# Performance work log

Measured on AMD Instinct MI355X. Metric: run time of the kernel, lower is better.

The kernel has to match this reference:

```python
import jax, jax.numpy as jnp
import numpy as np

N = 50000   # nodes
E = 800000  # edges (avg degree 16)
F_IN = 128
D_HID = 128
N_CLASS = 40


def setup_inputs() -> dict:
    key = jax.random.key(0)
    ks = jax.random.split(key, 10)
    s = 0.05
    return {
        "x": jax.random.normal(ks[0], (N, F_IN), jnp.float32),
        "edge_index": jax.random.randint(ks[1], (2, E), 0, N, dtype=jnp.int32),
        "W_in": jax.random.normal(ks[2], (F_IN, D_HID), jnp.float32) * s,
        "b_in": jnp.zeros((D_HID,), jnp.float32),
        "W1": jax.random.normal(ks[3], (D_HID, D_HID), jnp.float32) * s,
        "b1": jnp.zeros((D_HID,), jnp.float32),
        "W2": jax.random.normal(ks[4], (D_HID, D_HID), jnp.float32) * s,
        "b2": jnp.zeros((D_HID,), jnp.float32),
        "W_out": jax.random.normal(ks[5], (D_HID, N_CLASS), jnp.float32) * s,
        "b_out": jnp.zeros((N_CLASS,), jnp.float32),
    }


def _gcn_norm(edge_index, num_nodes):
    # Add self loops, compute symmetric normalization D^-1/2 (A+I) D^-1/2.
    loop = jnp.arange(num_nodes, dtype=edge_index.dtype)
    src = jnp.concatenate([edge_index[0], loop])
    dst = jnp.concatenate([edge_index[1], loop])
    deg = jnp.zeros((num_nodes,), jnp.float32).at[dst].add(1.0)
    dinv = jnp.where(deg > 0, jax.lax.rsqrt(deg), 0.0)
    norm = dinv[src] * dinv[dst]  # [E+N]
    return src, dst, norm


def _gcn_conv(h, W, b, src, dst, norm, num_nodes):
    # transform then sparse aggregate (gather-scale-scatter)
    h = h @ W                                   # [N, d]
    msg = h[src] * norm[:, None]                # [E+N, d]
    agg = jax.ops.segment_sum(msg, dst, num_segments=num_nodes)
    return agg + b


def reference(x, edge_index, W_in, b_in, W1, b1, W2, b2, W_out, b_out):
    num_nodes = x.shape[0]
    src, dst, norm = _gcn_norm(edge_index, num_nodes)
    h = _gcn_conv(x, W_in, b_in, src, dst, norm, num_nodes)
    # eval mode: dropout is identity
    h = jax.nn.relu(_gcn_conv(h, W1, b1, src, dst, norm, num_nodes))
    h = jax.nn.relu(_gcn_conv(h, W2, b2, src, dst, norm, num_nodes))
    out = h @ W_out + b_out
    return jax.nn.log_softmax(out, axis=1)
```

## Files before the change

### kernel.cpp

```cpp
#include <hip/hip_runtime.h>
#include <hip/hip_bf16.h>
#include <math.h>

#define NEG_INF (-3.402823466e38f)
typedef unsigned int uint;
typedef unsigned short ushort;
typedef __attribute__((ext_vector_type(8))) short short8;
typedef __attribute__((ext_vector_type(4))) float f32x4;

__device__ __forceinline__ float bf_lo(uint u) { return __uint_as_float(u << 16); }
__device__ __forceinline__ float bf_hi(uint u) { return __uint_as_float(u & 0xffff0000u); }
__device__ __forceinline__ ushort f2bf(float f) {
  __hip_bfloat16 h = __float2bfloat16(f);
  return *reinterpret_cast<ushort*>(&h);
}
__device__ __forceinline__ uint pack2(float a, float b) {
  return (uint)f2bf(a) | ((uint)f2bf(b) << 16);
}

__global__ __launch_bounds__(256) void k_pcnt(
    const float* __restrict__ W_in, const float* __restrict__ W1,
    const float* __restrict__ W2, ushort* __restrict__ Wt,
    const int* __restrict__ edges, int* __restrict__ cnt8, int E, int n)
{
  int b = blockIdx.x;
  if (b < 24) {
    const float* W = (b < 8) ? W_in : (b < 16) ? W1 : W2;
    ushort* dst = Wt + (size_t)(b >> 3) * 16384;
    int id = (b & 7) * 256 + threadIdx.x;
    int col = id >> 4, kc = id & 15;
    const float* src = W + (size_t)(kc * 8) * 128 + col;
    uint4 pk;
    pk.x = pack2(src[0],       src[128]);
    pk.y = pack2(src[2 * 128], src[3 * 128]);
    pk.z = pack2(src[4 * 128], src[5 * 128]);
    pk.w = pack2(src[6 * 128], src[7 * 128]);
    ((uint4*)dst)[id] = pk;
  } else {
    int cb = b - 24;
    int* my = cnt8 + (size_t)(cb & 7) * n;
    int stride = ((int)gridDim.x - 24) * 256;
    for (int e = cb * 256 + threadIdx.x; e < E; e += stride)
      atomicAdd(&my[edges[E + e]], 1);
  }
}

__global__ void k_scan1(const int* __restrict__ cnt8, int* __restrict__ cnt,
                        int* __restrict__ incl, int* __restrict__ bsum,
                        float* __restrict__ dinv, int n) {
  __shared__ int s[256];
  int tid = threadIdx.x;
  int gid = blockIdx.x * 256 + tid;
  int x = 0;
  if (gid < n) {
    #pragma unroll
    for (int p = 0; p < 8; ++p) x += cnt8[(size_t)p * n + gid];
    cnt[gid] = x;
    dinv[gid] = rsqrtf((float)x + 1.0f);
  }
  s[tid] = x;
  __syncthreads();
  #pragma unroll
  for (int off = 1; off < 256; off <<= 1) {
    int t = (tid >= off) ? s[tid - off] : 0;
    __syncthreads();
    x += t; s[tid] = x;
    __syncthreads();
  }
  incl[gid] = x;
  if (tid == 255) bsum[blockIdx.x] = x;
}

__global__ void k_scan3(const int* __restrict__ incl, const int* __restrict__ cnt,
                        const int* __restrict__ bsum, int* __restrict__ offs,
                        int* __restrict__ curs, int n, int E, int nb) {
  __shared__ int sb[256];
  int tid = threadIdx.x;
  sb[tid] = (tid < (int)blockIdx.x && tid < nb) ? bsum[tid] : 0;
  __syncthreads();
  #pragma unroll
  for (int off = 128; off; off >>= 1) {
    if (tid < off) sb[tid] += sb[tid + off];
    __syncthreads();
  }
  int base = sb[0];
  int gid = blockIdx.x * 256 + tid;
  if (gid < n) {
    int v = incl[gid] - cnt[gid] + base;
    offs[gid] = v;
    curs[gid] = v;
  }
  if (gid == 0) offs[n] = E;
}

__global__ __launch_bounds__(256) void k_gf(
    const float* __restrict__ A, const ushort* __restrict__ Wt,
    const float* __restrict__ dinv, ushort* __restrict__ T, int n, int fb,
    const int* __restrict__ edges, int* __restrict__ curs,
    int* __restrict__ csr, int E, int npp, int nbp)
{
  int tid = threadIdx.x;

  if ((int)blockIdx.x < fb) {
    int b2 = blockIdx.x;
    int part = b2 & 7;
    int lo = part * npp, hi = lo + npp;
    int stride = nbp * 256;
    int e = (b2 >> 3) * 256 + tid;
    for (; e + 3 * stride < E; e += 4 * stride) {
      int d0 = edges[E + e];
      int d1 = edges[E + e + stride];
      int d2 = edges[E + e + 2 * stride];
      int d3 = edges[E + e + 3 * stride];
      if (d0 >= lo && d0 < hi) { int s = edges[e];              csr[atomicAdd(&curs[d0], 1)] = s; }
      if (d1 >= lo && d1 < hi) { int s = edges[e + stride];     csr[atomicAdd(&curs[d1], 1)] = s; }
      if (d2 >= lo && d2 < hi) { int s = edges[e + 2 * stride]; csr[atomicAdd(&curs[d2], 1)] = s; }
      if (d3 >= lo && d3 < hi) { int s = edges[e + 3 * stride]; csr[atomicAdd(&curs[d3], 1)] = s; }
    }
    for (; e < E; e += stride) {
      int d = edges[E + e];
      if (d >= lo && d < hi) { int s = edges[e]; csr[atomicAdd(&curs[d], 1)] = s; }
    }
    return;
  }

  int wid = tid >> 6, lane = tid & 63;
  int lr = lane & 15, lg = lane >> 4;
  int rbase = ((int)blockIdx.x - fb) * 64 + wid * 16;
  int arow = rbase + lr;
  bool valid = arow < n;

  f32x4 acc[8];
  #pragma unroll
  for (int cf = 0; cf < 8; ++cf) acc[cf] = (f32x4){0.f, 0.f, 0.f, 0.f};

  #pragma unroll
  for (int ks = 0; ks < 4; ++ks) {
    short8 a = {};
    if (valid) {
      const float4* Af = (const float4*)(A + (size_t)arow * 128) + (ks * 4 + lg) * 2;
      float4 u = Af[0], w = Af[1];
      union { uint4 u4; short8 s8; } cv;
      cv.u4.x = pack2(u.x, u.y); cv.u4.y = pack2(u.z, u.w);
      cv.u4.z = pack2(w.x, w.y); cv.u4.w = pack2(w.z, w.w);
      a = cv.s8;
    }
    int kc = (ks << 2) | lg;
    #pragma unroll
    for (int cf = 0; cf < 8; ++cf) {
      int col = (cf << 4) | lr;
      const short8* bp = (const short8*)Wt + ((col << 4) | kc);
      acc[cf] = __builtin_amdgcn_mfma_f32_16x16x32_bf16(a, *bp, acc[cf], 0, 0, 0);
    }
  }

  #pragma unroll
  for (int v = 0; v < 4; ++v) {
    int row = rbase + (lg << 2) + v;
    if (row < n) {
      float s = dinv[row];
      ushort* dst = T + (size_t)row * 128 + lr;
      #pragma unroll
      for (int cf = 0; cf < 8; ++cf) dst[cf << 4] = f2bf(acc[cf][v] * s);
    }
  }
}

__global__ __launch_bounds__(256) void k_gemm(
    const ushort* __restrict__ Ap, const ushort* __restrict__ Wt,
    const float* __restrict__ dinv, ushort* __restrict__ T, int n)
{
  __shared__ ushort sW[128 * 128];
  int tid = threadIdx.x;
  {
    const uint4* Wt4 = (const uint4*)Wt;
    uint4* sW4 = (uint4*)sW;
    #pragma unroll
    for (int j = 0; j < 8; ++j) {
      int id = j * 256 + tid;
      int col = id >> 4, kc = id & 15;
      sW4[(col << 4) | (kc ^ (col & 7))] = Wt4[id];
    }
  }
  __syncthreads();

  int wid = tid >> 6, lane = tid & 63;
  int lr = lane & 15, lg = lane >> 4;
  int rbase = blockIdx.x * 64 + wid * 16;
  int arow = rbase + lr;
  bool valid = arow < n;

  f32x4 acc[8];
  #pragma unroll
  for (int cf = 0; cf < 8; ++cf) acc[cf] = (f32x4){0.f, 0.f, 0.f, 0.f};

  #pragma unroll
  for (int ks = 0; ks < 4; ++ks) {
    short8 a = {};
    if (valid) a = ((const short8*)(Ap + (size_t)arow * 128))[ks * 4 + lg];
    int kc = (ks << 2) | lg;
    #pragma unroll
    for (int cf = 0; cf < 8; ++cf) {
      int col = (cf << 4) | lr;
      const short8* bp = (const short8*)sW + ((col << 4) | (kc ^ (lr & 7)));
      acc[cf] = __builtin_amdgcn_mfma_f32_16x16x32_bf16(a, *bp, acc[cf], 0, 0, 0);
    }
  }

  #pragma unroll
  for (int v = 0; v < 4; ++v) {
    int row = rbase + (lg << 2) + v;
    if (row < n) {
      float s = dinv[row];
      ushort* dst = T + (size_t)row * 128 + lr;
      #pragma unroll
      for (int cf = 0; cf < 8; ++cf) dst[cf << 4] = f2bf(acc[cf][v] * s);
    }
  }
}

template <int RELU>
__global__ __launch_bounds__(256) void k_agg(
    const ushort* __restrict__ T, const int* __restrict__ offs,
    const int* __restrict__ csr, const float* __restrict__ dinv,
    const float* __restrict__ bias, ushort* __restrict__ H, int n)
{
  int u = (blockIdx.x << 2) + (threadIdx.x >> 6);
  if (u >= n) return;
  int lane = threadIdx.x & 63;
  const uint* Tu = (const uint*)T;
  uint su = Tu[(size_t)u * 64 + lane];
  float ax = bf_lo(su), ay = bf_hi(su);
  int e0 = offs[u], e1 = offs[u + 1];
  int deg = e1 - e0;
  int dcap = deg > 64 ? 64 : deg;
  int eid = (lane < deg) ? csr[e0 + lane] : 0;
  int j = 0;
  for (; j + 8 <= dcap; j += 8) {
    int s0 = __shfl(eid, j);     int s1 = __shfl(eid, j + 1);
    int s2 = __shfl(eid, j + 2); int s3 = __shfl(eid, j + 3);
    int s4 = __shfl(eid, j + 4); int s5 = __shfl(eid, j + 5);
    int s6 = __shfl(eid, j + 6); int s7 = __shfl(eid, j + 7);
    uint v0 = Tu[(size_t)s0 * 64 + lane];
    uint v1 = Tu[(size_t)s1 * 64 + lane];
    uint v2 = Tu[(size_t)s2 * 64 + lane];
    uint v3 = Tu[(size_t)s3 * 64 + lane];
    uint v4 = Tu[(size_t)s4 * 64 + lane];
    uint v5 = Tu[(size_t)s5 * 64 + lane];
    uint v6 = Tu[(size_t)s6 * 64 + lane];
    uint v7 = Tu[(size_t)s7 * 64 + lane];
    ax += ((bf_lo(v0) + bf_lo(v1)) + (bf_lo(v2) + bf_lo(v3))) +
          ((bf_lo(v4) + bf_lo(v5)) + (bf_lo(v6) + bf_lo(v7)));
    ay += ((bf_hi(v0) + bf_hi(v1)) + (bf_hi(v2) + bf_hi(v3))) +
          ((bf_hi(v4) + bf_hi(v5)) + (bf_hi(v6) + bf_hi(v7)));
  }
  for (; j < dcap; ++j) {
    int s = __shfl(eid, j);
    uint v = Tu[(size_t)s * 64 + lane];
    ax += bf_lo(v); ay += bf_hi(v);
  }
  for (int e = e0 + 64; e < e1; ++e) {
    uint v = Tu[(size_t)csr[e] * 64 + lane];
    ax += bf_lo(v); ay += bf_hi(v);
  }
  float du = dinv[u];
  float2 b2 = *(const float2*)(bias + (lane << 1));
  float ox = fmaf(ax, du, b2.x);
  float oy = fmaf(ay, du, b2.y);
  if (RELU) { ox = fmaxf(ox, 0.f); oy = fmaxf(oy, 0.f); }
  ((uint*)H)[(size_t)u * 64 + lane] = pack2(ox, oy);
}

__global__ __launch_bounds__(256) void k_head(
    const ushort* __restrict__ H, const float* __restrict__ Wo,
    const float* __restrict__ bo, float* __restrict__ out, int n)
{
  __shared__ float sWo[128 * 40];
  __shared__ float sX[128 * 64];
  int tid = threadIdx.x;
  int rbase = blockIdx.x * 64;

  {
    const float4* Wo4 = (const float4*)Wo;
    float4* sWo4 = (float4*)sWo;
    #pragma unroll
    for (int i = 0; i < 5; ++i) sWo4[i * 256 + tid] = Wo4[i * 256 + tid];
  }
  {
    const uint4* H4 = (const uint4*)H;
    #pragma unroll
    for (int j = 0; j < 4; ++j) {
      int id = j * 256 + tid;
      int r = id & 63, kc8 = id >> 6;
      int row = rbase + r;
      uint4 v = make_uint4(0u, 0u, 0u, 0u);
      if (row < n) v = H4[(size_t)row * 16 + kc8];
      float f[8] = {bf_lo(v.x), bf_hi(v.x), bf_lo(v.y), bf_hi(v.y),
                    bf_lo(v.z), bf_hi(v.z), bf_lo(v.w), bf_hi(v.w)};
      #pragma unroll
      for (int j2 = 0; j2 < 8; ++j2) {
        int k = kc8 * 8 + j2;
        int swz = ((k >> 2) & 7) << 2;
        sX[k * 64 + (r ^ swz)] = f[j2];
      }
    }
  }
  __syncthreads();

  int cg = tid & 7;
  int rg = tid >> 3;
  float bj[5];
  #pragma unroll
  for (int j = 0; j < 5; ++j) bj[j] = bo[cg * 5 + j];
  float acc[2][5];
  #pragma unroll
  for (int i = 0; i < 2; ++i)
    #pragma unroll
    for (int j = 0; j < 5; ++j) acc[i][j] = bj[j];

  #pragma unroll 4
  for (int k = 0; k < 128; ++k) {
    int swz = ((k >> 2) & 7) << 2;
    float2 xv = *(const float2*)(sX + k * 64 + ((rg << 1) ^ swz));
    const float* wr = sWo + k * 40 + cg * 5;
    float w0 = wr[0], w1 = wr[1], w2 = wr[2], w3 = wr[3], w4 = wr[4];
    acc[0][0] = fmaf(xv.x, w0, acc[0][0]);
    acc[0][1] = fmaf(xv.x, w1, acc[0][1]);
    acc[0][2] = fmaf(xv.x, w2, acc[0][2]);
    acc[0][3] = fmaf(xv.x, w3, acc[0][3]);
    acc[0][4] = fmaf(xv.x, w4, acc[0][4]);
    acc[1][0] = fmaf(xv.y, w0, acc[1][0]);
    acc[1][1] = fmaf(xv.y, w1, acc[1][1]);
    acc[1][2] = fmaf(xv.y, w2, acc[1][2]);
    acc[1][3] = fmaf(xv.y, w3, acc[1][3]);
    acc[1][4] = fmaf(xv.y, w4, acc[1][4]);
  }

  #pragma unroll
  for (int i = 0; i < 2; ++i) {
    int row = rbase + (rg << 1) + i;
    float m = acc[i][0];
    m = fmaxf(m, acc[i][1]); m = fmaxf(m, acc[i][2]);
    m = fmaxf(m, acc[i][3]); m = fmaxf(m, acc[i][4]);
    m = fmaxf(m, __shfl_xor(m, 1));
    m = fmaxf(m, __shfl_xor(m, 2));
    m = fmaxf(m, __shfl_xor(m, 4));
    float s = 0.f;
    #pragma unroll
    for (int j = 0; j < 5; ++j) s += __expf(acc[i][j] - m);
    s += __shfl_xor(s, 1);
    s += __shfl_xor(s, 2);
    s += __shfl_xor(s, 4);
    float ls = m + __logf(s);
    if (row < n) {
      float* dst = out + (size_t)row * 40 + cg * 5;
      #pragma unroll
      for (int j = 0; j < 5; ++j) dst[j] = acc[i][j] - ls;
    }
  }
}

extern "C" void kernel_launch(void* const* d_in, const int* in_sizes, int n_in,
                              void* d_out, int out_size, void* d_ws, size_t ws_size,
                              hipStream_t stream) {
  const float* x    = (const float*)d_in[0];
  const int*   edges= (const int*)d_in[1];
  const float* W_in = (const float*)d_in[2];
  const float* b_in = (const float*)d_in[3];
  const float* W1   = (const float*)d_in[4];
  const float* b1   = (const float*)d_in[5];
  const float* W2   = (const float*)d_in[6];
  const float* b2   = (const float*)d_in[7];
  const float* Wo   = (const float*)d_in[8];
  const float* bo   = (const float*)d_in[9];
  float* out = (float*)d_out;

  int N = in_sizes[0] / 128;
  int E = in_sizes[1] / 2;
  int NB = (N + 255) / 256;

  char* p = (char*)d_ws;
  auto alloc = [&](size_t bytes) {
    char* r = p; p += (bytes + 255) & ~(size_t)255; return r;
  };
  ushort* t   = (ushort*)alloc((size_t)N * 128 * 2);
  ushort* h   = (ushort*)alloc((size_t)N * 128 * 2);
  ushort* wt  = (ushort*)alloc(3 * 16384 * 2);
  int*   cnt8 = (int*)  alloc((size_t)N * 8 * 4);
  int*   cnt  = (int*)  alloc((size_t)N * 4);
  float* dinv = (float*)alloc((size_t)N * 4);
  int*   incl = (int*)  alloc((size_t)NB * 256 * 4);
  int*   bsum = (int*)  alloc(256 * 4);
  int*   offs = (int*)  alloc((size_t)(N + 1) * 4);
  int*   curs = (int*)  alloc((size_t)N * 4);
  int*   csr  = (int*)  alloc((size_t)E * 4);
  (void)ws_size; (void)n_in; (void)out_size;

  int NPP = (N + 7) / 8;
  int NBP = 512;
  int FB  = NBP * 8;
  int GB  = (N + 63) / 64;
  int AB  = (N + 3) / 4;

  hipMemsetAsync(cnt8, 0, (size_t)N * 8 * 4, stream);
  k_pcnt <<<24 + 2048, 256, 0, stream>>>(W_in, W1, W2, wt, edges, cnt8, E, N);
  k_scan1<<<NB, 256, 0, stream>>>(cnt8, cnt, incl, bsum, dinv, N);
  k_scan3<<<NB, 256, 0, stream>>>(incl, cnt, bsum, offs, curs, N, E, NB);
  k_gf   <<<FB + GB, 256, 0, stream>>>(x, wt, dinv, t, N, FB,
                                       edges, curs, csr, E, NPP, NBP);
  k_agg<0><<<AB, 256, 0, stream>>>(t, offs, csr, dinv, b_in, h, N);
  k_gemm <<<GB, 256, 0, stream>>>(h, wt + 16384, dinv, t, N);
  k_agg<1><<<AB, 256, 0, stream>>>(t, offs, csr, dinv, b1, h, N);
  k_gemm <<<GB, 256, 0, stream>>>(h, wt + 2 * 16384, dinv, t, N);
  k_agg<1><<<AB, 256, 0, stream>>>(t, offs, csr, dinv, b2, h, N);
  k_head <<<GB, 256, 0, stream>>>(h, Wo, bo, out, N);
}
```

Baseline: 251.2 us.

## Stage W in swizzled LDS for fused GEMM, reorder blocks, widen aggregation unroll

The fused GEMM/CSR-fill kernel now copies the 128x128 bf16 weight into shared memory with an XOR swizzle and reads MFMA B operands from LDS instead of global memory. GEMM blocks are placed first in the grid so they dispatch ahead of the CSR scatter blocks. The aggregation kernel unrolls neighbor gathers by 16 with a 4-wide tail, putting more loads in flight. Trade-offs are 32KB of LDS per block, which can lower occupancy and also applies to the scatter blocks, plus higher register pressure in aggregation.

```diff
diff --git a/kernel.cpp b/kernel.cpp
--- a/kernel.cpp
+++ b/kernel.cpp
@@ -95,14 +95,15 @@
 
 __global__ __launch_bounds__(256) void k_gf(
     const float* __restrict__ A, const ushort* __restrict__ Wt,
-    const float* __restrict__ dinv, ushort* __restrict__ T, int n, int fb,
+    const float* __restrict__ dinv, ushort* __restrict__ T, int n, int gb,
     const int* __restrict__ edges, int* __restrict__ curs,
     int* __restrict__ csr, int E, int npp, int nbp)
 {
+  __shared__ ushort sW[128 * 128];
   int tid = threadIdx.x;
 
-  if ((int)blockIdx.x < fb) {
-    int b2 = blockIdx.x;
+  if ((int)blockIdx.x >= gb) {
+    int b2 = blockIdx.x - gb;
     int part = b2 & 7;
     int lo = part * npp, hi = lo + npp;
     int stride = nbp * 256;
@@ -124,9 +125,21 @@
     return;
   }
 
+  {
+    const uint4* Wt4 = (const uint4*)Wt;
+    uint4* sW4 = (uint4*)sW;
+    #pragma unroll
+    for (int j = 0; j < 8; ++j) {
+      int id = j * 256 + tid;
+      int col = id >> 4, kc = id & 15;
+      sW4[(col << 4) | (kc ^ (col & 7))] = Wt4[id];
+    }
+  }
+  __syncthreads();
+
   int wid = tid >> 6, lane = tid & 63;
   int lr = lane & 15, lg = lane >> 4;
-  int rbase = ((int)blockIdx.x - fb) * 64 + wid * 16;
+  int rbase = blockIdx.x * 64 + wid * 16;
   int arow = rbase + lr;
   bool valid = arow < n;
 
@@ -149,7 +162,7 @@
     #pragma unroll
     for (int cf = 0; cf < 8; ++cf) {
       int col = (cf << 4) | lr;
-      const short8* bp = (const short8*)Wt + ((col << 4) | kc);
+      const short8* bp = (const short8*)sW + ((col << 4) | (kc ^ (lr & 7)));
       acc[cf] = __builtin_amdgcn_mfma_f32_16x16x32_bf16(a, *bp, acc[cf], 0, 0, 0);
     }
   }
@@ -236,23 +249,27 @@
   int dcap = deg > 64 ? 64 : deg;
   int eid = (lane < deg) ? csr[e0 + lane] : 0;
   int j = 0;
-  for (; j + 8 <= dcap; j += 8) {
+  for (; j + 16 <= dcap; j += 16) {
+    uint v[16];
+    #pragma unroll
+    for (int q = 0; q < 16; ++q) {
+      int s = __shfl(eid, j + q);
+      v[q] = Tu[(size_t)s * 64 + lane];
+    }
+    float sx = 0.f, sy = 0.f;
+    #pragma unroll
+    for (int q = 0; q < 16; ++q) { sx += bf_lo(v[q]); sy += bf_hi(v[q]); }
+    ax += sx; ay += sy;
+  }
+  for (; j + 4 <= dcap; j += 4) {
     int s0 = __shfl(eid, j);     int s1 = __shfl(eid, j + 1);
     int s2 = __shfl(eid, j + 2); int s3 = __shfl(eid, j + 3);
-    int s4 = __shfl(eid, j + 4); int s5 = __shfl(eid, j + 5);
-    int s6 = __shfl(eid, j + 6); int s7 = __shfl(eid, j + 7);
     uint v0 = Tu[(size_t)s0 * 64 + lane];
     uint v1 = Tu[(size_t)s1 * 64 + lane];
     uint v2 = Tu[(size_t)s2 * 64 + lane];
     uint v3 = Tu[(size_t)s3 * 64 + lane];
-    uint v4 = Tu[(size_t)s4 * 64 + lane];
-    uint v5 = Tu[(size_t)s5 * 64 + lane];
-    uint v6 = Tu[(size_t)s6 * 64 + lane];
-    uint v7 = Tu[(size_t)s7 * 64 + lane];
-    ax += ((bf_lo(v0) + bf_lo(v1)) + (bf_lo(v2) + bf_lo(v3))) +
-          ((bf_lo(v4) + bf_lo(v5)) + (bf_lo(v6) + bf_lo(v7)));
-    ay += ((bf_hi(v0) + bf_hi(v1)) + (bf_hi(v2) + bf_hi(v3))) +
-          ((bf_hi(v4) + bf_hi(v5)) + (bf_hi(v6) + bf_hi(v7)));
+    ax += (bf_lo(v0) + bf_lo(v1)) + (bf_lo(v2) + bf_lo(v3));
+    ay += (bf_hi(v0) + bf_hi(v1)) + (bf_hi(v2) + bf_hi(v3));
   }
   for (; j < dcap; ++j) {
     int s = __shfl(eid, j);
@@ -398,7 +415,6 @@
 
   int NPP = (N + 7) / 8;
   int NBP = 512;
-  int FB  = NBP * 8;
   int GB  = (N + 63) / 64;
   int AB  = (N + 3) / 4;
 
@@ -406,8 +422,8 @@
   k_pcnt <<<24 + 2048, 256, 0, stream>>>(W_in, W1, W2, wt, edges, cnt8, E, N);
   k_scan1<<<NB, 256, 0, stream>>>(cnt8, cnt, incl, bsum, dinv, N);
   k_scan3<<<NB, 256, 0, stream>>>(incl, cnt, bsum, offs, curs, N, E, NB);
-  k_gf   <<<FB + GB, 256, 0, stream>>>(x, wt, dinv, t, N, FB,
-                                       edges, curs, csr, E, NPP, NBP);
+  k_gf   <<<GB + NBP * 8, 256, 0, stream>>>(x, wt, dinv, t, N, GB,
+                                            edges, curs, csr, E, NPP, NBP);
   k_agg<0><<<AB, 256, 0, stream>>>(t, offs, csr, dinv, b_in, h, N);
   k_gemm <<<GB, 256, 0, stream>>>(h, wt + 16384, dinv, t, N);
   k_agg<1><<<AB, 256, 0, stream>>>(t, offs, csr, dinv, b1, h, N);
```

Measured after the change: 225.7 us. 10.1% less time.
